# Optimization experiments

Hardware: AMD Instinct MI355X
Metric: run time of the kernel (lower is better)

The kernel has to match this reference:

```python
import jax, jax.numpy as jnp
import numpy as np

D_MODEL = 1024
N_HEADS = 16
HEAD_DIM = D_MODEL // N_HEADS


def _linear_params(key, fan_in, fan_out):
    kw, kb = jax.random.split(key)
    bound = 1.0 / np.sqrt(fan_in)
    W = jax.random.uniform(kw, (fan_in, fan_out), jnp.float32, -bound, bound)
    b = jax.random.uniform(kb, (fan_out,), jnp.float32, -bound, bound)
    return W, b


def setup_inputs() -> dict:
    key = jax.random.key(0)
    ks = jax.random.split(key, 7)
    B, N = 4, 2048
    q = jax.random.normal(ks[0], (B, N, D_MODEL), jnp.float32)
    k = jax.random.normal(ks[1], (B, N, D_MODEL), jnp.float32)
    v = jax.random.normal(ks[2], (B, N, D_MODEL), jnp.float32)
    Wq, bq = _linear_params(ks[3], D_MODEL, D_MODEL)
    Wk, bk = _linear_params(ks[4], D_MODEL, D_MODEL)
    Wv, bv = _linear_params(ks[5], D_MODEL, D_MODEL)
    Wo, bo = _linear_params(ks[6], D_MODEL, D_MODEL)
    return {"q": q, "k": k, "v": v,
            "Wq": Wq, "bq": bq, "Wk": Wk, "bk": bk,
            "Wv": Wv, "bv": bv, "Wo": Wo, "bo": bo}


def reference(q, k, v, Wq, bq, Wk, bk, Wv, bv, Wo, bo):
    B, N, _ = q.shape
    # fused QKV projection + head split: [B, N, D] -> [B, H, N, hd]
    def split_heads(x):
        return x.reshape(B, N, N_HEADS, HEAD_DIM).transpose(0, 2, 1, 3)
    qh = split_heads(q @ Wq + bq)
    kh = split_heads(k @ Wk + bk)
    vh = split_heads(v @ Wv + bv)
    # scaled dot-product attention (mask=None)
    scale = 1.0 / np.sqrt(HEAD_DIM)
    scores = jnp.einsum('bhqd,bhkd->bhqk', qh, kh) * scale  # [B,H,N,N]
    attn_weights = jax.nn.softmax(scores, axis=-1)
    attn_out = jnp.einsum('bhqk,bhkd->bhqd', attn_weights, vh)
    # merge heads: [B,H,N,hd] -> [B,N,D]
    attn_out = attn_out.transpose(0, 2, 1, 3).reshape(B, N, D_MODEL)
    output = attn_out @ Wo + bo
    return output, attn_weights
```

## Files before the change

kernel.cpp:

```cpp
#include <hip/hip_runtime.h>
#include <hip/hip_bf16.h>
#include <stdint.h>

#define D_MODEL 1024
#define NH      16
#define HD      64
#define B_SZ    4
#define SEQ     2048
#define M_TOT   (B_SZ*SEQ)
#define LOG2E_O8 0.18033688011112042f

typedef __bf16 bf16;
typedef bf16  bf16x8 __attribute__((ext_vector_type(8)));
typedef bf16  bf16x4 __attribute__((ext_vector_type(4)));
typedef float f32x4  __attribute__((ext_vector_type(4)));

static __device__ __forceinline__ f32x4 mfma16(bf16x8 a, bf16x8 b, f32x4 c) {
  return __builtin_amdgcn_mfma_f32_16x16x32_bf16(a, b, c, 0, 0, 0);
}

static __device__ __forceinline__ void gl2lds(const void* g, void* l) {
  __builtin_amdgcn_global_load_lds(
      (const __attribute__((address_space(1))) unsigned int*)g,
      (__attribute__((address_space(3))) unsigned int*)l,
      16, 0, 0);
}

#define BAR_VM16() do { \
  asm volatile("s_waitcnt vmcnt(16) lgkmcnt(0)" ::: "memory"); \
  __builtin_amdgcn_s_barrier(); \
  __builtin_amdgcn_sched_barrier(0); \
} while (0)

#define BAR_LGKM() do { \
  asm volatile("s_waitcnt lgkmcnt(0)" ::: "memory"); \
  __builtin_amdgcn_s_barrier(); \
  __builtin_amdgcn_sched_barrier(0); \
} while (0)

static __device__ __forceinline__ int lds_off(int r, int kb) {
  return ((r >> 1) << 7) + ((((r & 1) << 6) + kb) ^ (((r >> 1) & 7) << 4));
}

__global__ __launch_bounds__(256) void k_twt(const float* __restrict__ w0,
                                             const float* __restrict__ w1,
                                             const float* __restrict__ w2,
                                             const float* __restrict__ w3,
                                             bf16* __restrict__ t0,
                                             bf16* __restrict__ t1,
                                             bf16* __restrict__ t2,
                                             bf16* __restrict__ t3) {
  __shared__ bf16 t[64][65];
  int z = blockIdx.z;
  const float* W = z == 0 ? w0 : z == 1 ? w1 : z == 2 ? w2 : w3;
  bf16* Wt = z == 0 ? t0 : z == 1 ? t1 : z == 2 ? t2 : t3;
  int k0 = blockIdx.x * 64, n0 = blockIdx.y * 64;
  int r = threadIdx.x >> 2, c0 = (threadIdx.x & 3) * 16;
  const float* p = W + (size_t)(k0 + r) * D_MODEL + n0 + c0;
#pragma unroll
  for (int e = 0; e < 16; e += 4) {
    float4 v = *(const float4*)(p + e);
    t[r][c0+e+0] = (bf16)v.x; t[r][c0+e+1] = (bf16)v.y;
    t[r][c0+e+2] = (bf16)v.z; t[r][c0+e+3] = (bf16)v.w;
  }
  __syncthreads();
  bf16x8 o0, o1;
#pragma unroll
  for (int e = 0; e < 8; e++) { o0[e] = t[c0+e][r]; o1[e] = t[c0+8+e][r]; }
  bf16* q = Wt + (size_t)(n0 + r) * D_MODEL + k0 + c0;
  *(bf16x8*)q = o0; *(bf16x8*)(q + 8) = o1;
}

__global__ __launch_bounds__(256, 2) void k_qkv8(const float* __restrict__ Aq,
                                                 const float* __restrict__ Ak,
                                                 const float* __restrict__ Av,
                                                 const bf16* __restrict__ Wt3,
                                                 const float* __restrict__ bq,
                                                 const float* __restrict__ bk,
                                                 const float* __restrict__ bv,
                                                 bf16* __restrict__ HQ,
                                                 bf16* __restrict__ Vt) {
  __shared__ alignas(16) char smem[73728];
  const int tid = threadIdx.x;
  const int lane = tid & 63, wv = tid >> 6;
  const int g = lane >> 4, lr = lane & 15;
  const int wm = wv >> 1, wn = wv & 1;
  const int dd = blockIdx.x;
  const int P = (dd & 7) * 96 + (dd >> 3);
  const int seg = P >> 8;
  const int rem = P & 255;
  const int m0 = (rem >> 2) * 128;
  const int n0 = (rem & 3) * 256;

  const float* A = seg == 0 ? Aq : seg == 1 ? Ak : Av;
  const float* bias = seg == 0 ? bq : seg == 1 ? bk : bv;
  const float oscale = seg == 0 ? LOG2E_O8 : 1.0f;

  const float* aptr = A + (size_t)(m0 + (tid >> 1)) * D_MODEL + (tid & 1) * 16;
  const int awoff0 = lds_off(tid >> 1, (tid & 1) * 32);
  const int awoff1 = lds_off(tid >> 1, (tid & 1) * 32 + 16);
  const char* bsrc[4]; int bdst[4];
#pragma unroll
  for (int u = 0; u < 4; u++) {
    int o = u * 4096 + tid * 16;
    int p = o >> 7, w = o & 127;
    int wq = w ^ ((p & 7) << 4);
    int r = p * 2 + (wq >> 6), kb = wq & 63;
    bsrc[u] = (const char*)(Wt3 + (size_t)(seg * 1024 + n0 + r) * D_MODEL) + kb;
    bdst[u] = o;
  }
  int aoff[4], boff[8];
#pragma unroll
  for (int mi = 0; mi < 4; mi++) aoff[mi] = lds_off(wm * 64 + mi * 16 + lr, g * 16);
#pragma unroll
  for (int ni = 0; ni < 8; ni++) boff[ni] = lds_off(wn * 128 + ni * 16 + lr, g * 16);

  f32x4 acc[4][8] = {};
  float4 af[4];

#pragma unroll
  for (int j = 0; j < 4; j++) af[j] = *(const float4*)(aptr + j * 4);
#pragma unroll
  for (int u = 0; u < 4; u++) gl2lds(bsrc[u], smem + 24576 + bdst[u]);
  asm volatile("s_waitcnt vmcnt(0)" ::: "memory");
  {
    bf16x8 w8a, w8b;
#pragma unroll
    for (int e = 0; e < 4; e++) {
      w8a[e] = (bf16)af[0][e]; w8a[4+e] = (bf16)af[1][e];
      w8b[e] = (bf16)af[2][e]; w8b[4+e] = (bf16)af[3][e];
    }
    *(bf16x8*)(smem + awoff0) = w8a;
    *(bf16x8*)(smem + awoff1) = w8b;
  }

  int bufc = 0;
  for (int s = 0; s < 32; ++s) {
    int kn = (s + 1) & 31;
    int nxt = bufc + 1; if (nxt == 3) nxt = 0;
#pragma unroll
    for (int j = 0; j < 4; j++) af[j] = *(const float4*)(aptr + kn * 32 + j * 4);
#pragma unroll
    for (int u = 0; u < 4; u++)
      gl2lds(bsrc[u] + kn * 64, smem + 24576 + nxt * 16384 + bdst[u]);
    asm volatile("s_waitcnt vmcnt(8) lgkmcnt(0)" ::: "memory");
    __builtin_amdgcn_s_barrier();
    __builtin_amdgcn_sched_barrier(0);
    const char* bA = smem + bufc * 8192;
    const char* bB = smem + 24576 + bufc * 16384;
    bf16x8 a[4], b[8];
#pragma unroll
    for (int mi = 0; mi < 4; mi++) a[mi] = *(const bf16x8*)(bA + aoff[mi]);
#pragma unroll
    for (int ni = 0; ni < 8; ni++) b[ni] = *(const bf16x8*)(bB + boff[ni]);
#pragma unroll
    for (int mi = 0; mi < 4; mi++)
#pragma unroll
      for (int ni = 0; ni < 8; ni++)
        acc[mi][ni] = mfma16(a[mi], b[ni], acc[mi][ni]);
    {
      bf16x8 w8a, w8b;
#pragma unroll
      for (int e = 0; e < 4; e++) {
        w8a[e] = (bf16)af[0][e]; w8a[4+e] = (bf16)af[1][e];
        w8b[e] = (bf16)af[2][e]; w8b[4+e] = (bf16)af[3][e];
      }
      *(bf16x8*)(smem + nxt * 8192 + awoff0) = w8a;
      *(bf16x8*)(smem + nxt * 8192 + awoff1) = w8b;
    }
    bufc = nxt;
  }

  if (seg < 2) {
    bf16* outp = HQ + (size_t)seg * 8388608;
#pragma unroll
    for (int mi = 0; mi < 4; mi++) {
#pragma unroll
      for (int ni = 0; ni < 8; ni++) {
        int n = n0 + wn * 128 + ni * 16 + lr;
        float bvl = bias[n];
        int h = n >> 6, dcol = n & 63;
#pragma unroll
        for (int r = 0; r < 4; r++) {
          int m = m0 + wm * 64 + mi * 16 + g * 4 + r;
          int b2 = m >> 11, q = m & 2047;
          outp[(((size_t)(b2 * NH + h)) * SEQ + q) * HD + dcol] =
              (bf16)((acc[mi][ni][r] + bvl) * oscale);
        }
      }
    }
  } else {
    __syncthreads();
    char* tr = smem;
#pragma unroll
    for (int mi = 0; mi < 4; mi++) {
#pragma unroll
      for (int ni = 0; ni < 8; ni++) {
        int n_loc = wn * 128 + ni * 16 + lr;
        float bvl = bias[n0 + n_loc];
        bf16x4 pq;
#pragma unroll
        for (int r = 0; r < 4; r++) pq[r] = (bf16)(acc[mi][ni][r] + bvl);
        int m0l = wm * 64 + mi * 16 + g * 4;
        *(bf16x4*)(tr + n_loc * 256 + ((m0l * 2) ^ ((n_loc & 7) << 4))) = pq;
      }
    }
    __syncthreads();
    int n_loc = tid;
    int n_glob = n0 + n_loc;
    int h = n_glob >> 6, dcol = n_glob & 63;
    int b2 = m0 >> 11, q0l = m0 & 2047;
    bf16* vp = Vt + ((size_t)(b2 * NH + h) * HD + dcol) * SEQ + q0l;
    int sw = (n_loc & 7) << 4;
#pragma unroll
    for (int c = 0; c < 16; c++) {
      bf16x8 v8 = *(const bf16x8*)(tr + n_loc * 256 + ((c * 16) ^ sw));
      *(bf16x8*)(vp + c * 8) = v8;
    }
  }
}

__global__ __launch_bounds__(256) void k_ogemm(const bf16* __restrict__ A,
                                               const bf16* __restrict__ Bt,
                                               const float* __restrict__ bias,
                                               float* __restrict__ outp) {
  __shared__ alignas(16) bf16 sA[2][8192];
  __shared__ alignas(16) bf16 sB[2][8192];
  const int tid = threadIdx.x;
  const int lane = tid & 63, wv = tid >> 6;
  const int g = lane >> 4, lr = lane & 15;
  const int wm = wv >> 1, wn = wv & 1;
  const int d = blockIdx.x;
  const int m0 = ((d & 7) * 8 + (d >> 6)) * 128;
  const int n0 = ((d >> 3) & 7) * 128;

  const char* asrc[4]; const char* bsrc[4]; int dst[4];
#pragma unroll
  for (int i = 0; i < 4; i++) {
    int o = i * 4096 + tid * 16;
    int row = o >> 7, in = o & 127;
    int cs = in ^ ((row & 7) << 4);
    asrc[i] = (const char*)A  + (size_t)(m0 + row) * 2048 + cs;
    bsrc[i] = (const char*)Bt + (size_t)(n0 + row) * 2048 + cs;
    dst[i] = i * 4096 + wv * 1024;
  }
  int fa[4], fb[4], swa[4], swb[4];
#pragma unroll
  for (int i = 0; i < 4; i++) {
    int rowa = wm * 64 + i * 16 + lr;
    int rowb = wn * 64 + i * 16 + lr;
    fa[i] = rowa * 128; swa[i] = (rowa & 7) << 4;
    fb[i] = rowb * 128; swb[i] = (rowb & 7) << 4;
  }
  f32x4 acc[4][4] = {};
#pragma unroll
  for (int i = 0; i < 4; i++) {
    gl2lds(asrc[i], (char*)sA[0] + dst[i]);
    gl2lds(bsrc[i], (char*)sB[0] + dst[i]);
  }
  __syncthreads();
  int cur = 0;
  for (int kt = 0; kt < 16; ++kt) {
    if (kt < 15) {
#pragma unroll
      for (int i = 0; i < 4; i++) {
        gl2lds(asrc[i] + (kt + 1) * 128, (char*)sA[cur ^ 1] + dst[i]);
        gl2lds(bsrc[i] + (kt + 1) * 128, (char*)sB[cur ^ 1] + dst[i]);
      }
    }
    const char* bA = (const char*)sA[cur];
    const char* bB = (const char*)sB[cur];
#pragma unroll
    for (int c = 0; c < 2; c++) {
      bf16x8 a[4], b[4];
      int off = c * 64 + g * 16;
#pragma unroll
      for (int i = 0; i < 4; i++) {
        a[i] = *(const bf16x8*)(bA + fa[i] + (off ^ swa[i]));
        b[i] = *(const bf16x8*)(bB + fb[i] + (off ^ swb[i]));
      }
#pragma unroll
      for (int mi = 0; mi < 4; mi++)
#pragma unroll
        for (int ni = 0; ni < 4; ni++)
          acc[mi][ni] = mfma16(a[mi], b[ni], acc[mi][ni]);
    }
    __syncthreads();
    cur ^= 1;
  }
#pragma unroll
  for (int mi = 0; mi < 4; mi++) {
#pragma unroll
    for (int ni = 0; ni < 4; ni++) {
      int n = n0 + wn * 64 + ni * 16 + lr;
      float bvl = bias[n];
#pragma unroll
      for (int r = 0; r < 4; r++) {
        int m = m0 + wm * 64 + mi * 16 + g * 4 + r;
        outp[(size_t)m * D_MODEL + n] = acc[mi][ni][r] + bvl;
      }
    }
  }
}

__global__ __launch_bounds__(256) void k_attn(const bf16* __restrict__ Qh,
                                              const bf16* __restrict__ Kh,
                                              const bf16* __restrict__ Vt,
                                              float* __restrict__ Wout,
                                              bf16* __restrict__ O) {
  __shared__ alignas(16) bf16 sK[2][8192];
  __shared__ alignas(16) bf16 sV[8192];
  __shared__ alignas(16) bf16 sP[16384];
  const int tid = threadIdx.x, lane = tid & 63, wv = tid >> 6;
  const int g = lane >> 4, lr = lane & 15;
  int swzb = (blockIdx.x & 7) * 64 + (blockIdx.x >> 3);
  const int bh = swzb >> 3;
  const int qt0 = (swzb & 7) * 256;
  const int qw0 = qt0 + wv * 32;
  const int qw1 = qt0 + 128 + wv * 32;

  bf16x8 qb0[2][2], qb1[2][2];
#pragma unroll
  for (int mi = 0; mi < 2; mi++)
#pragma unroll
    for (int c = 0; c < 2; c++) {
      qb0[mi][c] = *(const bf16x8*)(Qh + ((size_t)bh * SEQ + qw0 + mi * 16 + lr) * HD + c * 32 + g * 8);
      qb1[mi][c] = *(const bf16x8*)(Qh + ((size_t)bh * SEQ + qw1 + mi * 16 + lr) * HD + c * 32 + g * 8);
    }

  const char* kbase = (const char*)(Kh + (size_t)bh * SEQ * HD);
  const char* vbase = (const char*)(Vt + (size_t)bh * HD * SEQ);
  const char* ksrc[4]; const char* vsrc[4]; int ldst[4];
#pragma unroll
  for (int i = 0; i < 4; i++) {
    int o = i * 4096 + tid * 16;
    int kr = o >> 7, kin = o & 127;
    ksrc[i] = kbase + (size_t)kr * 128 + (kin ^ ((kr & 7) << 4));
    int dr = o >> 8, vin = o & 255;
    vsrc[i] = vbase + (size_t)dr * 4096 + (vin ^ ((dr & 7) << 4));
    ldst[i] = i * 4096 + wv * 1024;
  }

#pragma unroll
  for (int i = 0; i < 4; i++) gl2lds(ksrc[i], (char*)sK + ldst[i]);
  __syncthreads();

  float rsum0[2] = {0.f, 0.f};
  int cur = 0;
  for (int kt = 0; kt < 16; ++kt) {
    int nx = ((kt + 1) & 15) * 16384;
#pragma unroll
    for (int i = 0; i < 4; i++)
      gl2lds(ksrc[i] + nx, (char*)sK + (cur ^ 1) * 16384 + ldst[i]);
    const char* kb = (char*)sK + cur * 16384;
#pragma unroll
    for (int nf = 0; nf < 8; nf++) {
      int krow = nf * 16 + lr, sw = (krow & 7) << 4;
      bf16x8 k0 = *(const bf16x8*)(kb + krow * 128 + ((g * 16) ^ sw));
      bf16x8 k1 = *(const bf16x8*)(kb + krow * 128 + ((64 + g * 16) ^ sw));
#pragma unroll
      for (int mi = 0; mi < 2; mi++) {
        f32x4 t = {};
        t = mfma16(k0, qb0[mi][0], t);
        t = mfma16(k1, qb0[mi][1], t);
        rsum0[mi] += __builtin_amdgcn_exp2f(t[0]) + __builtin_amdgcn_exp2f(t[1])
                   + __builtin_amdgcn_exp2f(t[2]) + __builtin_amdgcn_exp2f(t[3]);
      }
    }
    __syncthreads();
    cur ^= 1;
  }
  float lrl0[2];
#pragma unroll
  for (int mi = 0; mi < 2; mi++) {
    float s = rsum0[mi];
    s += __shfl_xor(s, 16); s += __shfl_xor(s, 32);
    lrl0[mi] = -__builtin_amdgcn_logf(s);
  }
  const int osrc0 = (lane >> 3) + 16 * (lane & 3);
  const int osrc1 = 8 + (lane >> 3) + 16 * (lane & 3);
  const bool selhi = (lane >> 2) & 1;
  float* wrow0[2][2]; float* wrow1[2][2];
#pragma unroll
  for (int mi = 0; mi < 2; mi++)
#pragma unroll
    for (int h = 0; h < 2; h++) {
      wrow0[mi][h] = Wout + ((size_t)bh * SEQ + qw0 + mi * 16 + 8 * h + (lane >> 3)) * SEQ
                     + 4 * (lane & 7);
      wrow1[mi][h] = Wout + ((size_t)bh * SEQ + qw1 + mi * 16 + 8 * h + (lane >> 3)) * SEQ
                     + 4 * (lane & 7);
    }

  float rsum1[2] = {0.f, 0.f};
  f32x4 oc0[2][4] = {};
  for (int kt = 0; kt < 16; ++kt) {
#pragma unroll
    for (int i = 0; i < 4; i++) {
      gl2lds(ksrc[i] + ((kt + 1) & 15) * 16384, (char*)sK + (cur ^ 1) * 16384 + ldst[i]);
      gl2lds(vsrc[i] + kt * 256, (char*)sV + ldst[i]);
    }
    const char* kb = (char*)sK + cur * 16384;
#pragma unroll
    for (int mi = 0; mi < 2; mi++) {
      f32x4 wreg[8];
#pragma unroll
      for (int nf = 0; nf < 8; nf++) {
        int krow = nf * 16 + lr, sw = (krow & 7) << 4;
        bf16x8 k0 = *(const bf16x8*)(kb + krow * 128 + ((g * 16) ^ sw));
        bf16x8 k1 = *(const bf16x8*)(kb + krow * 128 + ((64 + g * 16) ^ sw));
        f32x4 t = {};
        t = mfma16(k0, qb0[mi][0], t);
        t = mfma16(k1, qb0[mi][1], t);
        f32x4 w4;
        w4[0] = __builtin_amdgcn_exp2f(t[0] + lrl0[mi]);
        w4[1] = __builtin_amdgcn_exp2f(t[1] + lrl0[mi]);
        w4[2] = __builtin_amdgcn_exp2f(t[2] + lrl0[mi]);
        w4[3] = __builtin_amdgcn_exp2f(t[3] + lrl0[mi]);
        wreg[nf] = w4;
        bf16x4 p4;
        p4[0] = (bf16)w4[0]; p4[1] = (bf16)w4[1]; p4[2] = (bf16)w4[2]; p4[3] = (bf16)w4[3];
        int lq = wv * 32 + mi * 16 + lr;
        *(bf16x4*)((char*)sP + lq * 256 + (((nf * 16 + g * 4) * 2) ^ ((lq & 7) << 4))) = p4;
      }
#pragma unroll
      for (int h = 0; h < 2; h++) {
        int osrc = h ? osrc1 : osrc0;
#pragma unroll
        for (int c = 0; c < 4; c++) {
          f32x4 va, vb, outv;
#pragma unroll
          for (int e = 0; e < 4; e++) {
            va[e] = __shfl(wreg[2 * c][e], osrc);
            vb[e] = __shfl(wreg[2 * c + 1][e], osrc);
          }
#pragma unroll
          for (int e = 0; e < 4; e++) outv[e] = selhi ? vb[e] : va[e];
          __builtin_nontemporal_store(outv,
              (f32x4*)(wrow0[mi][h] + kt * 128 + 32 * c));
        }
      }
    }
#pragma unroll
    for (int nf = 0; nf < 8; nf++) {
      int krow = nf * 16 + lr, sw = (krow & 7) << 4;
      bf16x8 k0 = *(const bf16x8*)(kb + krow * 128 + ((g * 16) ^ sw));
      bf16x8 k1 = *(const bf16x8*)(kb + krow * 128 + ((64 + g * 16) ^ sw));
#pragma unroll
      for (int mi = 0; mi < 2; mi++) {
        f32x4 t = {};
        t = mfma16(k0, qb1[mi][0], t);
        t = mfma16(k1, qb1[mi][1], t);
        rsum1[mi] += __builtin_amdgcn_exp2f(t[0]) + __builtin_amdgcn_exp2f(t[1])
                   + __builtin_amdgcn_exp2f(t[2]) + __builtin_amdgcn_exp2f(t[3]);
      }
    }
    BAR_VM16();
#pragma unroll
    for (int c = 0; c < 4; c++) {
      bf16x8 pa[2];
#pragma unroll
      for (int mi = 0; mi < 2; mi++) {
        int lq = wv * 32 + mi * 16 + lr;
        pa[mi] = *(const bf16x8*)((char*)sP + lq * 256 + ((c * 64 + g * 16) ^ ((lq & 7) << 4)));
      }
#pragma unroll
      for (int df = 0; df < 4; df++) {
        int dr = df * 16 + lr;
        bf16x8 vb2 = *(const bf16x8*)((char*)sV + dr * 256 + ((c * 64 + g * 16) ^ ((dr & 7) << 4)));
#pragma unroll
        for (int mi = 0; mi < 2; mi++)
          oc0[mi][df] = mfma16(pa[mi], vb2, oc0[mi][df]);
      }
    }
    BAR_LGKM();
    cur ^= 1;
  }
  float lrl1[2];
#pragma unroll
  for (int mi = 0; mi < 2; mi++) {
    float s = rsum1[mi];
    s += __shfl_xor(s, 16); s += __shfl_xor(s, 32);
    lrl1[mi] = -__builtin_amdgcn_logf(s);
  }
  {
    int b = bh >> 4, h = bh & 15;
#pragma unroll
    for (int mi = 0; mi < 2; mi++)
#pragma unroll
      for (int df = 0; df < 4; df++)
#pragma unroll
        for (int r = 0; r < 4; r++) {
          int q = qw0 + mi * 16 + g * 4 + r;
          int dcol = df * 16 + lr;
          O[((size_t)(b * SEQ + q) * NH + h) * HD + dcol] = (bf16)oc0[mi][df][r];
        }
  }

  f32x4 oc1[2][4] = {};
  for (int kt = 0; kt < 16; ++kt) {
#pragma unroll
    for (int i = 0; i < 4; i++) {
      if (kt < 15)
        gl2lds(ksrc[i] + (kt + 1) * 16384, (char*)sK + (cur ^ 1) * 16384 + ldst[i]);
      gl2lds(vsrc[i] + kt * 256, (char*)sV + ldst[i]);
    }
    const char* kb = (char*)sK + cur * 16384;
#pragma unroll
    for (int mi = 0; mi < 2; mi++) {
      f32x4 wreg[8];
#pragma unroll
      for (int nf = 0; nf < 8; nf++) {
        int krow = nf * 16 + lr, sw = (krow & 7) << 4;
        bf16x8 k0 = *(const bf16x8*)(kb + krow * 128 + ((g * 16) ^ sw));
        bf16x8 k1 = *(const bf16x8*)(kb + krow * 128 + ((64 + g * 16) ^ sw));
        f32x4 t = {};
        t = mfma16(k0, qb1[mi][0], t);
        t = mfma16(k1, qb1[mi][1], t);
        f32x4 w4;
        w4[0] = __builtin_amdgcn_exp2f(t[0] + lrl1[mi]);
        w4[1] = __builtin_amdgcn_exp2f(t[1] + lrl1[mi]);
        w4[2] = __builtin_amdgcn_exp2f(t[2] + lrl1[mi]);
        w4[3] = __builtin_amdgcn_exp2f(t[3] + lrl1[mi]);
        wreg[nf] = w4;
        bf16x4 p4;
        p4[0] = (bf16)w4[0]; p4[1] = (bf16)w4[1]; p4[2] = (bf16)w4[2]; p4[3] = (bf16)w4[3];
        int lq = wv * 32 + mi * 16 + lr;
        *(bf16x4*)((char*)sP + lq * 256 + (((nf * 16 + g * 4) * 2) ^ ((lq & 7) << 4))) = p4;
      }
#pragma unroll
      for (int h = 0; h < 2; h++) {
        int osrc = h ? osrc1 : osrc0;
#pragma unroll
        for (int c = 0; c < 4; c++) {
          f32x4 va, vb, outv;
#pragma unroll
          for (int e = 0; e < 4; e++) {
            va[e] = __shfl(wreg[2 * c][e], osrc);
            vb[e] = __shfl(wreg[2 * c + 1][e], osrc);
          }
#pragma unroll
          for (int e = 0; e < 4; e++) outv[e] = selhi ? vb[e] : va[e];
          __builtin_nontemporal_store(outv,
              (f32x4*)(wrow1[mi][h] + kt * 128 + 32 * c));
        }
      }
    }
    BAR_VM16();
#pragma unroll
    for (int c = 0; c < 4; c++) {
      bf16x8 pa[2];
#pragma unroll
      for (int mi = 0; mi < 2; mi++) {
        int lq = wv * 32 + mi * 16 + lr;
        pa[mi] = *(const bf16x8*)((char*)sP + lq * 256 + ((c * 64 + g * 16) ^ ((lq & 7) << 4)));
      }
#pragma unroll
      for (int df = 0; df < 4; df++) {
        int dr = df * 16 + lr;
        bf16x8 vb2 = *(const bf16x8*)((char*)sV + dr * 256 + ((c * 64 + g * 16) ^ ((dr & 7) << 4)));
#pragma unroll
        for (int mi = 0; mi < 2; mi++)
          oc1[mi][df] = mfma16(pa[mi], vb2, oc1[mi][df]);
      }
    }
    BAR_LGKM();
    cur ^= 1;
  }
  {
    int b = bh >> 4, h = bh & 15;
#pragma unroll
    for (int mi = 0; mi < 2; mi++)
#pragma unroll
      for (int df = 0; df < 4; df++)
#pragma unroll
        for (int r = 0; r < 4; r++) {
          int q = qw1 + mi * 16 + g * 4 + r;
          int dcol = df * 16 + lr;
          O[((size_t)(b * SEQ + q) * NH + h) * HD + dcol] = (bf16)oc1[mi][df][r];
        }
  }
}

extern "C" void kernel_launch(void* const* d_in, const int* in_sizes, int n_in,
                              void* d_out, int out_size, void* d_ws, size_t ws_size,
                              hipStream_t stream) {
  const float* q  = (const float*)d_in[0];
  const float* k  = (const float*)d_in[1];
  const float* v  = (const float*)d_in[2];
  const float* Wq = (const float*)d_in[3];
  const float* bq = (const float*)d_in[4];
  const float* Wk = (const float*)d_in[5];
  const float* bk = (const float*)d_in[6];
  const float* Wv = (const float*)d_in[7];
  const float* bv = (const float*)d_in[8];
  const float* Wo = (const float*)d_in[9];
  const float* bo = (const float*)d_in[10];

  char* ws = (char*)d_ws;
  bf16* Obuf = (bf16*)(ws);
  bf16* Wt3  = (bf16*)(ws + 16777216);
  bf16* WtO  = (bf16*)(ws + 16777216 + 3 * 2097152);
  bf16* HQ   = (bf16*)(ws + 25165824);
  bf16* Kh   = (bf16*)(ws + 41943040);
  bf16* Vt   = (bf16*)(ws + 75497472);

  float* out0 = (float*)d_out;
  float* wout = out0 + (size_t)M_TOT * D_MODEL;

  dim3 blk(256);
  k_twt<<<dim3(16, 16, 4), blk, 0, stream>>>(Wq, Wk, Wv, Wo,
                                             Wt3, Wt3 + 1048576, Wt3 + 2097152, WtO);
  k_qkv8<<<dim3(768), blk, 0, stream>>>(q, k, v, Wt3, bq, bk, bv, HQ, Vt);
  k_attn<<<dim3(512), blk, 0, stream>>>(HQ, Kh, Vt, wout, Obuf);
  k_ogemm<<<dim3(512), blk, 0, stream>>>(Obuf, WtO, bo, out0);
}
```

Before: 348.0 us.

## Retile output GEMM to 128x256 tiles with finer k-steps and explicit waitcnt pipelining

Replaces the 128x128 output-projection GEMM with a 128x256-tile kernel running 256 blocks, with each wave computing a 64x128 sub-tile. The K loop now takes 32-element steps using a packed two-rows-per-128-byte swizzled LDS layout. Double buffering is driven by explicit vmcnt/lgkmcnt waits and raw barriers instead of __syncthreads. The larger tile increases operand reuse and cuts global traffic for the weight matrix. The cost is fewer blocks to fill the GPU and more accumulator registers per thread.

```diff
diff --git a/kernel.cpp b/kernel.cpp
--- a/kernel.cpp
+++ b/kernel.cpp
@@ -220,79 +220,85 @@
   }
 }
 
-__global__ __launch_bounds__(256) void k_ogemm(const bf16* __restrict__ A,
-                                               const bf16* __restrict__ Bt,
-                                               const float* __restrict__ bias,
-                                               float* __restrict__ outp) {
-  __shared__ alignas(16) bf16 sA[2][8192];
-  __shared__ alignas(16) bf16 sB[2][8192];
+__global__ __launch_bounds__(256, 2) void k_ogemm8(const bf16* __restrict__ A,
+                                                   const bf16* __restrict__ Bt,
+                                                   const float* __restrict__ bias,
+                                                   float* __restrict__ outp) {
+  __shared__ alignas(16) char smem[49152];
   const int tid = threadIdx.x;
   const int lane = tid & 63, wv = tid >> 6;
   const int g = lane >> 4, lr = lane & 15;
   const int wm = wv >> 1, wn = wv & 1;
-  const int d = blockIdx.x;
-  const int m0 = ((d & 7) * 8 + (d >> 6)) * 128;
-  const int n0 = ((d >> 3) & 7) * 128;
-
-  const char* asrc[4]; const char* bsrc[4]; int dst[4];
-#pragma unroll
-  for (int i = 0; i < 4; i++) {
-    int o = i * 4096 + tid * 16;
-    int row = o >> 7, in = o & 127;
-    int cs = in ^ ((row & 7) << 4);
-    asrc[i] = (const char*)A  + (size_t)(m0 + row) * 2048 + cs;
-    bsrc[i] = (const char*)Bt + (size_t)(n0 + row) * 2048 + cs;
-    dst[i] = i * 4096 + wv * 1024;
-  }
-  int fa[4], fb[4], swa[4], swb[4];
-#pragma unroll
-  for (int i = 0; i < 4; i++) {
-    int rowa = wm * 64 + i * 16 + lr;
-    int rowb = wn * 64 + i * 16 + lr;
-    fa[i] = rowa * 128; swa[i] = (rowa & 7) << 4;
-    fb[i] = rowb * 128; swb[i] = (rowb & 7) << 4;
-  }
-  f32x4 acc[4][4] = {};
-#pragma unroll
-  for (int i = 0; i < 4; i++) {
-    gl2lds(asrc[i], (char*)sA[0] + dst[i]);
-    gl2lds(bsrc[i], (char*)sB[0] + dst[i]);
-  }
-  __syncthreads();
+  const int dd = blockIdx.x;
+  const int P = (dd & 7) * 32 + (dd >> 3);
+  const int m0 = (P >> 2) * 128;
+  const int n0 = (P & 3) * 256;
+
+  const char* asrc[2]; int adst[2];
+#pragma unroll
+  for (int u = 0; u < 2; u++) {
+    int o = u * 4096 + tid * 16;
+    int p = o >> 7, w = o & 127;
+    int wq = w ^ ((p & 7) << 4);
+    int r = p * 2 + (wq >> 6), kb = wq & 63;
+    asrc[u] = (const char*)(A + (size_t)(m0 + r) * D_MODEL) + kb;
+    adst[u] = o;
+  }
+  const char* bsrc[4]; int bdst[4];
+#pragma unroll
+  for (int u = 0; u < 4; u++) {
+    int o = u * 4096 + tid * 16;
+    int p = o >> 7, w = o & 127;
+    int wq = w ^ ((p & 7) << 4);
+    int r = p * 2 + (wq >> 6), kb = wq & 63;
+    bsrc[u] = (const char*)(Bt + (size_t)(n0 + r) * D_MODEL) + kb;
+    bdst[u] = o;
+  }
+  int aoff[4], boff[8];
+#pragma unroll
+  for (int mi = 0; mi < 4; mi++) aoff[mi] = lds_off(wm * 64 + mi * 16 + lr, g * 16);
+#pragma unroll
+  for (int ni = 0; ni < 8; ni++) boff[ni] = lds_off(wn * 128 + ni * 16 + lr, g * 16);
+
+  f32x4 acc[4][8] = {};
+#pragma unroll
+  for (int u = 0; u < 2; u++) gl2lds(asrc[u], smem + adst[u]);
+#pragma unroll
+  for (int u = 0; u < 4; u++) gl2lds(bsrc[u], smem + 16384 + bdst[u]);
+
   int cur = 0;
-  for (int kt = 0; kt < 16; ++kt) {
-    if (kt < 15) {
-#pragma unroll
-      for (int i = 0; i < 4; i++) {
-        gl2lds(asrc[i] + (kt + 1) * 128, (char*)sA[cur ^ 1] + dst[i]);
-        gl2lds(bsrc[i] + (kt + 1) * 128, (char*)sB[cur ^ 1] + dst[i]);
-      }
-    }
-    const char* bA = (const char*)sA[cur];
-    const char* bB = (const char*)sB[cur];
-#pragma unroll
-    for (int c = 0; c < 2; c++) {
-      bf16x8 a[4], b[4];
-      int off = c * 64 + g * 16;
-#pragma unroll
-      for (int i = 0; i < 4; i++) {
-        a[i] = *(const bf16x8*)(bA + fa[i] + (off ^ swa[i]));
-        b[i] = *(const bf16x8*)(bB + fb[i] + (off ^ swb[i]));
-      }
-#pragma unroll
-      for (int mi = 0; mi < 4; mi++)
-#pragma unroll
-        for (int ni = 0; ni < 4; ni++)
-          acc[mi][ni] = mfma16(a[mi], b[ni], acc[mi][ni]);
-    }
-    __syncthreads();
+  for (int s = 0; s < 32; ++s) {
+    int kn = (s + 1) & 31;
+#pragma unroll
+    for (int u = 0; u < 2; u++)
+      gl2lds(asrc[u] + kn * 64, smem + (cur ^ 1) * 8192 + adst[u]);
+#pragma unroll
+    for (int u = 0; u < 4; u++)
+      gl2lds(bsrc[u] + kn * 64, smem + 16384 + (cur ^ 1) * 16384 + bdst[u]);
+    asm volatile("s_waitcnt vmcnt(6)" ::: "memory");
+    __builtin_amdgcn_s_barrier();
+    __builtin_amdgcn_sched_barrier(0);
+    const char* bA = smem + cur * 8192;
+    const char* bB = smem + 16384 + cur * 16384;
+    bf16x8 a[4], b[8];
+#pragma unroll
+    for (int mi = 0; mi < 4; mi++) a[mi] = *(const bf16x8*)(bA + aoff[mi]);
+#pragma unroll
+    for (int ni = 0; ni < 8; ni++) b[ni] = *(const bf16x8*)(bB + boff[ni]);
+#pragma unroll
+    for (int mi = 0; mi < 4; mi++)
+#pragma unroll
+      for (int ni = 0; ni < 8; ni++)
+        acc[mi][ni] = mfma16(a[mi], b[ni], acc[mi][ni]);
+    asm volatile("s_waitcnt lgkmcnt(0)" ::: "memory");
+    __builtin_amdgcn_s_barrier();
     cur ^= 1;
   }
 #pragma unroll
   for (int mi = 0; mi < 4; mi++) {
 #pragma unroll
-    for (int ni = 0; ni < 4; ni++) {
-      int n = n0 + wn * 64 + ni * 16 + lr;
+    for (int ni = 0; ni < 8; ni++) {
+      int n = n0 + wn * 128 + ni * 16 + lr;
       float bvl = bias[n];
 #pragma unroll
       for (int r = 0; r < 4; r++) {
@@ -612,5 +618,5 @@
                                              Wt3, Wt3 + 1048576, Wt3 + 2097152, WtO);
   k_qkv8<<<dim3(768), blk, 0, stream>>>(q, k, v, Wt3, bq, bk, bv, HQ, Vt);
   k_attn<<<dim3(512), blk, 0, stream>>>(HQ, Kh, Vt, wout, Obuf);
-  k_ogemm<<<dim3(512), blk, 0, stream>>>(Obuf, WtO, bo, out0);
-}
+  k_ogemm8<<<dim3(256), blk, 0, stream>>>(Obuf, WtO, bo, out0);
+}
```

New measurement: 354.4 us. No clear change (+1.8%).
